# Kernel optimization log

Measured on AMD Instinct MI355X. Metric: run time of the kernel, lower is better.

## Reference

```python
import jax, jax.numpy as jnp
import numpy as np

B, T, I, H, O = 64, 512, 512, 1024, 128
EPS = 1e-5

def _uniform(key, shape, bound):
    return jax.random.uniform(key, shape, jnp.float32, -bound, bound)

def setup_inputs() -> dict:
    key = jax.random.key(0)
    ks = jax.random.split(key, 16)
    bI = 1.0 / np.sqrt(I)
    bH = 1.0 / np.sqrt(H)
    inp = {
        "x": jax.random.normal(ks[0], (B, T, I), jnp.float32),
        # input projection (Linear: y = x @ W.T + b)
        "w_proj": _uniform(ks[1], (H, I), bI),
        "b_proj": _uniform(ks[2], (H,), bI),
        # GRU layer 0 (input_dim -> hidden_dim), PyTorch gate order [r, z, n]
        "w_ih0": _uniform(ks[3], (3 * H, I), bH),
        "w_hh0": _uniform(ks[4], (3 * H, H), bH),
        "b_ih0": _uniform(ks[5], (3 * H,), bH),
        "b_hh0": _uniform(ks[6], (3 * H,), bH),
        # GRU layer 1 (hidden_dim -> hidden_dim)
        "w_ih1": _uniform(ks[7], (3 * H, H), bH),
        "w_hh1": _uniform(ks[8], (3 * H, H), bH),
        "b_ih1": _uniform(ks[9], (3 * H,), bH),
        "b_hh1": _uniform(ks[10], (3 * H,), bH),
        # BatchNorm1d (eval mode: running stats)
        "bn_gamma": jnp.ones((H,), jnp.float32),
        "bn_beta": jnp.zeros((H,), jnp.float32),
        "bn_mean": jnp.zeros((H,), jnp.float32),
        "bn_var": jnp.ones((H,), jnp.float32),
        # output projection
        "w_out": _uniform(ks[11], (O, H), bH),
        "b_out": _uniform(ks[12], (O,), bH),
    }
    return inp

def _gru_layer(x_seq, w_ih, w_hh, b_ih, b_hh):
    """x_seq: [B, T, D_in] -> outputs [B, T, H]. PyTorch GRU gate math."""
    # Precompute input-side gates for all timesteps in one big GEMM.
    gx = jnp.einsum('btd,gd->btg', x_seq, w_ih) + b_ih      # [B, T, 3H]
    gx = jnp.transpose(gx, (1, 0, 2))                        # [T, B, 3H]
    h0 = jnp.zeros((x_seq.shape[0], w_hh.shape[1]), x_seq.dtype)

    def step(h, gx_t):
        gh = h @ w_hh.T + b_hh                               # [B, 3H]
        gxr, gxz, gxn = jnp.split(gx_t, 3, axis=-1)
        ghr, ghz, ghn = jnp.split(gh, 3, axis=-1)
        r = jax.nn.sigmoid(gxr + ghr)
        z = jax.nn.sigmoid(gxz + ghz)
        n = jnp.tanh(gxn + r * ghn)
        h_new = (1.0 - z) * n + z * h
        return h_new, h_new

    _, ys = jax.lax.scan(step, h0, gx)                       # ys: [T, B, H]
    return jnp.transpose(ys, (1, 0, 2))                      # [B, T, H]

def reference(x, w_proj, b_proj,
              w_ih0, w_hh0, b_ih0, b_hh0,
              w_ih1, w_hh1, b_ih1, b_hh1,
              bn_gamma, bn_beta, bn_mean, bn_var,
              w_out, b_out):
    x_projected = x @ w_proj.T + b_proj                      # [B, T, H]
    h1 = _gru_layer(x, w_ih0, w_hh0, b_ih0, b_hh0)           # layer 0
    gru_out = _gru_layer(h1, w_ih1, w_hh1, b_ih1, b_hh1)     # layer 1 (eval: no inter-layer dropout)
    residual = x_projected + gru_out
    out = residual[:, -1, :]                                 # [B, H]
    # BatchNorm1d in eval mode (running stats); dropout is identity in eval.
    out = (out - bn_mean) * jax.lax.rsqrt(bn_var + EPS) * bn_gamma + bn_beta
    out = out @ w_out.T + b_out                              # [B, O]
    return out
```

## Files before the change

### kernel.cpp

```cpp
#include <hip/hip_runtime.h>
#include <math.h>

#define BB 64
#define TT 512
#define II 512
#define HH 1024
#define OO 128
#define GN (3*HH)
#define TC 64
#define NCH (TT/TC)
#define NSLOT 66

using u16 = unsigned short;
typedef __attribute__((ext_vector_type(8))) short bf16x8;
typedef __attribute__((ext_vector_type(4))) float f32x4;
typedef __attribute__((ext_vector_type(4))) unsigned short u16x4;

__device__ __forceinline__ u16 f2bf(float f){
  unsigned u = __builtin_bit_cast(unsigned, f);
  u += 0x7fffu + ((u >> 16) & 1u);
  return (u16)(u >> 16);
}
__device__ __forceinline__ float bf2f(u16 h){
  unsigned u = ((unsigned)h) << 16;
  return __builtin_bit_cast(float, u);
}

__global__ __launch_bounds__(256) void cvt_kernel(const float* __restrict__ s,
                                                  u16* __restrict__ d, int n4){
  int stride = gridDim.x * 256;
  for (int i = blockIdx.x * 256 + threadIdx.x; i < n4; i += stride){
    float4 v = reinterpret_cast<const float4*>(s)[i];
    u16x4 o; o.x = f2bf(v.x); o.y = f2bf(v.y); o.z = f2bf(v.z); o.w = f2bf(v.w);
    reinterpret_cast<u16x4*>(d)[i] = o;
  }
}

__global__ __launch_bounds__(256) void cvtx_chunk(const float* __restrict__ x,
                                                  u16* __restrict__ d, int t0){
  const int per_b = TC * II / 4;
  int stride = gridDim.x * 256;
  for (int i = blockIdx.x * 256 + threadIdx.x; i < BB * per_b; i += stride){
    int b = i / per_b, r = i - b * per_b;
    float4 v = reinterpret_cast<const float4*>(x)[(size_t)(b * TT + t0) * (II/4) + r];
    u16x4 o; o.x = f2bf(v.x); o.y = f2bf(v.y); o.z = f2bf(v.z); o.w = f2bf(v.w);
    reinterpret_cast<u16x4*>(d)[(size_t)b * per_b + r] = o;
  }
}

template<int K>
__global__ __launch_bounds__(256) void gemm_bias(const u16* __restrict__ A,
    const u16* __restrict__ Bw, const float* __restrict__ bias, u16* __restrict__ C){
  __shared__ u16 As[128*32];
  __shared__ u16 Bs[128*32];
  int tid = threadIdx.x;
  int lane = tid & 63, wave = tid >> 6;
  int m0 = blockIdx.x * 128, n0 = blockIdx.y * 128;
  int wr = (wave >> 1) * 64, wc = (wave & 1) * 64;
  int fr = lane & 15, fo = (lane >> 4) * 8;
  f32x4 acc[4][4] = {};
  for (int k0 = 0; k0 < K; k0 += 32){
    __syncthreads();
    #pragma unroll
    for (int c = 0; c < 2; ++c){
      int chunk = wave * 2 + c;
      int s = chunk * 64 + lane;
      int row = s >> 2, o = s & 3;
      const u16* ga = A  + (size_t)(m0 + row) * K + k0 + o * 8;
      const u16* gb = Bw + (size_t)(n0 + row) * K + k0 + o * 8;
      __builtin_amdgcn_global_load_lds(
          (const __attribute__((address_space(1))) unsigned int*)ga,
          (__attribute__((address_space(3))) unsigned int*)(As + chunk * 512), 16, 0, 0);
      __builtin_amdgcn_global_load_lds(
          (const __attribute__((address_space(1))) unsigned int*)gb,
          (__attribute__((address_space(3))) unsigned int*)(Bs + chunk * 512), 16, 0, 0);
    }
    __syncthreads();
    bf16x8 af[4], bf[4];
    #pragma unroll
    for (int m = 0; m < 4; ++m)
      af[m] = *reinterpret_cast<const bf16x8*>(&As[(wr + m*16 + fr) * 32 + fo]);
    #pragma unroll
    for (int n = 0; n < 4; ++n)
      bf[n] = *reinterpret_cast<const bf16x8*>(&Bs[(wc + n*16 + fr) * 32 + fo]);
    #pragma unroll
    for (int m = 0; m < 4; ++m)
      #pragma unroll
      for (int n = 0; n < 4; ++n)
        acc[m][n] = __builtin_amdgcn_mfma_f32_16x16x32_bf16(af[m], bf[n], acc[m][n], 0, 0, 0);
  }
  int r4 = (lane >> 4) * 4;
  #pragma unroll
  for (int n = 0; n < 4; ++n){
    int col = n0 + wc + n*16 + fr;
    float bv = bias[col];
    #pragma unroll
    for (int m = 0; m < 4; ++m){
      #pragma unroll
      for (int q = 0; q < 4; ++q){
        int row = m0 + wr + m*16 + r4 + q;
        C[(size_t)row * GN + col] = f2bf(acc[m][n][q] + bv);
      }
    }
  }
}

__device__ __forceinline__ void gru_chunk(
    const u16* __restrict__ gx, const u16* __restrict__ Whh, const float* __restrict__ bhh,
    u16* hbuf, unsigned* flags, u16* h1c, float* hstate, int base,
    int bl, u16* Ws, float* part, float* bsh)
{
  int tid = threadIdx.x, lane = tid & 63, w = tid >> 6;
  int g = bl >> 6, wg = bl & 63;
  int c0 = wg * 16, rb0 = g * 32;
  for (int ch = tid; ch < 48 * 128; ch += 256){
    int r = ch >> 7, o = ch & 127;
    const u16* src = Whh + (size_t)((r >> 4) * HH + c0 + (r & 15)) * HH + o * 8;
    *reinterpret_cast<int4*>(&Ws[r * 1032 + o * 8]) = *reinterpret_cast<const int4*>(src);
  }
  if (tid < 48) bsh[tid] = bhh[(tid >> 4) * HH + c0 + (tid & 15)];
  __syncthreads();
  int b2 = tid >> 4, j = tid & 15;
  int fr = lane & 15, klo = (lane >> 4) * 8, kw = w * 256;
  const u16* gxp0 = gx + (size_t)(rb0 + b2) * TC * GN + c0 + j;
  const u16* gxp1 = gx + (size_t)(rb0 + 16 + b2) * TC * GN + c0 + j;
  unsigned* fgrp = flags + g * 1024;
  float ho0 = hstate[(size_t)(rb0 + b2) * HH + c0 + j];
  float ho1 = hstate[(size_t)(rb0 + 16 + b2) * HH + c0 + j];
  int lnD = (b2 >> 2) * 16 + j, regD = b2 & 3;
  float br = bhh[c0 + j];
  for (int tl = 0; tl < TC; ++tl){
    int t = base + tl;
    float gxr0 = bf2f(gxp0[(size_t)tl * GN]);
    float gxz0 = bf2f(gxp0[(size_t)tl * GN + HH]);
    float gxn0 = bf2f(gxp0[(size_t)tl * GN + 2 * HH]);
    float gxr1 = bf2f(gxp1[(size_t)tl * GN]);
    float gxz1 = bf2f(gxp1[(size_t)tl * GN + HH]);
    float gxn1 = bf2f(gxp1[(size_t)tl * GN + 2 * HH]);
    if (tl){
      for (;;){
        unsigned v = __hip_atomic_load(fgrp + lane * 16, __ATOMIC_RELAXED,
                                       __HIP_MEMORY_SCOPE_AGENT);
        if (__all((int)(v >= (unsigned)tl))) break;
        __builtin_amdgcn_s_sleep(1);
      }
    }
    asm volatile("" ::: "memory");
    const u16* rslot = hbuf + (size_t)(((t - 1) % 65) + 1) * (BB * HH);
    const u16* hr0 = rslot + (size_t)(rb0 + fr) * HH + kw + klo;
    const u16* hr1 = hr0 + (size_t)16 * HH;
    bf16x8 af0[8], af1[8];
    #pragma unroll
    for (int ks = 0; ks < 8; ++ks){
      af0[ks] = *reinterpret_cast<const bf16x8*>(hr0 + ks * 32);
      af1[ks] = *reinterpret_cast<const bf16x8*>(hr1 + ks * 32);
    }
    f32x4 acc[2][3] = {};
    #pragma unroll
    for (int ks = 0; ks < 8; ++ks){
      int kk = kw + ks * 32 + klo;
      bf16x8 w0 = *reinterpret_cast<const bf16x8*>(&Ws[(      fr) * 1032 + kk]);
      bf16x8 w1 = *reinterpret_cast<const bf16x8*>(&Ws[(16 + fr) * 1032 + kk]);
      bf16x8 w2 = *reinterpret_cast<const bf16x8*>(&Ws[(32 + fr) * 1032 + kk]);
      acc[0][0] = __builtin_amdgcn_mfma_f32_16x16x32_bf16(af0[ks], w0, acc[0][0], 0, 0, 0);
      acc[0][1] = __builtin_amdgcn_mfma_f32_16x16x32_bf16(af0[ks], w1, acc[0][1], 0, 0, 0);
      acc[0][2] = __builtin_amdgcn_mfma_f32_16x16x32_bf16(af0[ks], w2, acc[0][2], 0, 0, 0);
      acc[1][0] = __builtin_amdgcn_mfma_f32_16x16x32_bf16(af1[ks], w0, acc[1][0], 0, 0, 0);
      acc[1][1] = __builtin_amdgcn_mfma_f32_16x16x32_bf16(af1[ks], w1, acc[1][1], 0, 0, 0);
      acc[1][2] = __builtin_amdgcn_mfma_f32_16x16x32_bf16(af1[ks], w2, acc[1][2], 0, 0, 0);
    }
    #pragma unroll
    for (int at = 0; at < 2; ++at)
      #pragma unroll
      for (int gt = 0; gt < 3; ++gt)
        *reinterpret_cast<f32x4*>(&part[((w*6 + at*3 + gt)*64 + lane)*4]) = acc[at][gt];
    __syncthreads();
    float gh[2][3];
    #pragma unroll
    for (int at = 0; at < 2; ++at)
      #pragma unroll
      for (int gt = 0; gt < 3; ++gt){
        float s = 0.f;
        #pragma unroll
        for (int ww = 0; ww < 4; ++ww)
          s += part[((ww*6 + at*3 + gt)*64 + lnD)*4 + regD];
        gh[at][gt] = s;
      }
    float bz = bsh[16 + j], bn2 = bsh[32 + j];
    float r0 = __builtin_amdgcn_rcpf(1.f + __expf(-(gxr0 + gh[0][0] + br)));
    float z0 = __builtin_amdgcn_rcpf(1.f + __expf(-(gxz0 + gh[0][1] + bz)));
    float nx0 = gxn0 + r0 * (gh[0][2] + bn2);
    float n0 = 1.f - 2.f * __builtin_amdgcn_rcpf(__expf(2.f * nx0) + 1.f);
    float hn0 = (1.f - z0) * n0 + z0 * ho0;
    float r1 = __builtin_amdgcn_rcpf(1.f + __expf(-(gxr1 + gh[1][0] + br)));
    float z1 = __builtin_amdgcn_rcpf(1.f + __expf(-(gxz1 + gh[1][1] + bz)));
    float nx1 = gxn1 + r1 * (gh[1][2] + bn2);
    float n1 = 1.f - 2.f * __builtin_amdgcn_rcpf(__expf(2.f * nx1) + 1.f);
    float hn1 = (1.f - z1) * n1 + z1 * ho1;
    ho0 = hn0; ho1 = hn1;
    u16 hb0 = f2bf(hn0), hb1 = f2bf(hn1);
    u16* wslot = hbuf + (size_t)((t % 65) + 1) * (BB * HH);
    size_t d0 = (size_t)(rb0 + b2) * HH + c0 + j;
    __hip_atomic_store(wslot + d0,                hb0, __ATOMIC_RELAXED, __HIP_MEMORY_SCOPE_AGENT);
    __hip_atomic_store(wslot + d0 + (size_t)16*HH, hb1, __ATOMIC_RELAXED, __HIP_MEMORY_SCOPE_AGENT);
    if (h1c){
      h1c[((size_t)(rb0 + b2) * TC + tl) * HH + c0 + j] = hb0;
      h1c[((size_t)(rb0 + 16 + b2) * TC + tl) * HH + c0 + j] = hb1;
    }
    if (tl == TC - 1){
      hstate[(size_t)(rb0 + b2) * HH + c0 + j] = hn0;
      hstate[(size_t)(rb0 + 16 + b2) * HH + c0 + j] = hn1;
    }
    __syncthreads();
    if (tid == 0)
      __hip_atomic_store(fgrp + wg * 16, (unsigned)(tl + 1), __ATOMIC_RELAXED,
                         __HIP_MEMORY_SCOPE_AGENT);
  }
}

__global__ __launch_bounds__(256, 1) void gru_fused(
    const u16* gxA, const u16* WhhA, const float* bhhA, u16* hbufA,
    unsigned* flA, u16* h1cA, float* hstA, int baseA,
    const u16* gxB, const u16* WhhB, const float* bhhB, u16* hbufB,
    unsigned* flB, float* hstB, int baseB)
{
  __shared__ u16 Ws[48 * 1032];
  __shared__ float part[4*6*64*4];
  __shared__ float bsh[48];
  int blk = blockIdx.x;
  if (blk < 128){
    if (!gxA) return;
    gru_chunk(gxA, WhhA, bhhA, hbufA, flA, h1cA, hstA, baseA, blk, Ws, part, bsh);
  } else {
    if (!gxB) return;
    gru_chunk(gxB, WhhB, bhhB, hbufB, flB, nullptr, hstB, baseB, blk - 128, Ws, part, bsh);
  }
}

__global__ __launch_bounds__(256) void xproj_kernel(const float* __restrict__ x,
    const float* __restrict__ wproj, const float* __restrict__ bproj, float* __restrict__ xp){
  __shared__ float xs[II];
  int b = blockIdx.x >> 2, n0 = (blockIdx.x & 3) << 8;
  const float* xrow = x + ((size_t)b * TT + (TT - 1)) * II;
  for (int i = threadIdx.x; i < II; i += 256) xs[i] = xrow[i];
  __syncthreads();
  int n = n0 + threadIdx.x;
  const float* wrow = wproj + (size_t)n * II;
  float s = 0.f;
  #pragma unroll 4
  for (int k = 0; k < II; k += 4){
    float4 w4 = *reinterpret_cast<const float4*>(&wrow[k]);
    s += xs[k]*w4.x + xs[k+1]*w4.y + xs[k+2]*w4.z + xs[k+3]*w4.w;
  }
  xp[(size_t)b * HH + n] = s + bproj[n];
}

__global__ __launch_bounds__(256) void final_kernel(const float* __restrict__ xp,
    const float* __restrict__ hl, const float* __restrict__ gamma, const float* __restrict__ beta,
    const float* __restrict__ mean, const float* __restrict__ var,
    const float* __restrict__ wout, const float* __restrict__ bout, float* __restrict__ out){
  __shared__ float bn[2 * HH];
  int b0 = blockIdx.x * 2;
  for (int i = threadIdx.x; i < 2 * HH; i += 256){
    int bb = i >> 10, jj = i & (HH - 1);
    float res = xp[(size_t)(b0 + bb) * HH + jj] + hl[(size_t)(b0 + bb) * HH + jj];
    bn[i] = (res - mean[jj]) * rsqrtf(var[jj] + 1e-5f) * gamma[jj] + beta[jj];
  }
  __syncthreads();
  int bb = threadIdx.x >> 7, o = threadIdx.x & (OO - 1);
  const float* wrow = wout + (size_t)o * HH;
  const float* bnrow = bn + bb * HH;
  float s = 0.f;
  #pragma unroll 4
  for (int k = 0; k < HH; k += 4){
    float4 w4 = *reinterpret_cast<const float4*>(&wrow[k]);
    s += bnrow[k]*w4.x + bnrow[k+1]*w4.y + bnrow[k+2]*w4.z + bnrow[k+3]*w4.w;
  }
  out[(size_t)(b0 + bb) * OO + o] = s + bout[o];
}

extern "C" void kernel_launch(void* const* d_in, const int* in_sizes, int n_in,
                              void* d_out, int out_size, void* d_ws, size_t ws_size,
                              hipStream_t stream) {
  const float* x      = (const float*)d_in[0];
  const float* w_proj = (const float*)d_in[1];
  const float* b_proj = (const float*)d_in[2];
  const float* w_ih0  = (const float*)d_in[3];
  const float* w_hh0  = (const float*)d_in[4];
  const float* b_ih0  = (const float*)d_in[5];
  const float* b_hh0  = (const float*)d_in[6];
  const float* w_ih1  = (const float*)d_in[7];
  const float* w_hh1  = (const float*)d_in[8];
  const float* b_ih1  = (const float*)d_in[9];
  const float* b_hh1  = (const float*)d_in[10];
  const float* gamma  = (const float*)d_in[11];
  const float* beta   = (const float*)d_in[12];
  const float* mean   = (const float*)d_in[13];
  const float* var    = (const float*)d_in[14];
  const float* w_out  = (const float*)d_in[15];
  const float* b_out  = (const float*)d_in[16];
  float* out = (float*)d_out;

  char* ws = (char*)d_ws;
  size_t off = 0;
  unsigned* flags = (unsigned*)(ws + off); off += (size_t)18 * 2048 * 4;
  float* hst0  = (float*)(ws + off); off += (size_t)BB*HH*4;
  float* hst1  = (float*)(ws + off); off += (size_t)BB*HH*4;
  size_t zeroA = off;
  u16* hbuf0   = (u16*)(ws + off);   off += (size_t)NSLOT*BB*HH*2;
  u16* hbuf1   = (u16*)(ws + off);   off += (size_t)NSLOT*BB*HH*2;
  float* xproj = (float*)(ws + off); off += (size_t)BB*HH*4;
  u16* xck     = (u16*)(ws + off);   off += (size_t)BB*TC*II*2;
  u16* h1c     = (u16*)(ws + off);   off += (size_t)BB*TC*HH*2;
  u16* wih0b   = (u16*)(ws + off);   off += (size_t)3*HH*II*2;
  u16* whh0b   = (u16*)(ws + off);   off += (size_t)3*HH*HH*2;
  u16* wih1b   = (u16*)(ws + off);   off += (size_t)3*HH*HH*2;
  u16* whh1b   = (u16*)(ws + off);   off += (size_t)3*HH*HH*2;
  u16* gxc0    = (u16*)(ws + off);   off += (size_t)BB*TC*3*HH*2;
  u16* gxc1    = (u16*)(ws + off);   off += (size_t)BB*TC*3*HH*2;

  hipMemsetAsync(d_ws, 0, zeroA, stream);
  hipMemsetAsync(hbuf0, 0, (size_t)BB*HH*2, stream);
  hipMemsetAsync(hbuf1, 0, (size_t)BB*HH*2, stream);

  cvt_kernel<<<512, 256, 0, stream>>>(w_ih0, wih0b, (3*HH*II) / 4);
  cvt_kernel<<<512, 256, 0, stream>>>(w_hh0, whh0b, (3*HH*HH) / 4);
  cvt_kernel<<<512, 256, 0, stream>>>(w_ih1, wih1b, (3*HH*HH) / 4);
  cvt_kernel<<<512, 256, 0, stream>>>(w_hh1, whh1b, (3*HH*HH) / 4);

  xproj_kernel<<<256, 256, 0, stream>>>(x, w_proj, b_proj, xproj);

  dim3 ggrid(BB * TC / 128, GN / 128);
  auto fl = [&](int k, int role){ return flags + (size_t)(k*2 + role) * 2048; };

  cvtx_chunk<<<1024, 256, 0, stream>>>(x, xck, 0);
  gemm_bias<II><<<ggrid, 256, 0, stream>>>(xck, wih0b, b_ih0, gxc0);
  gru_fused<<<256, 256, 0, stream>>>(gxc0, whh0b, b_hh0, hbuf0, fl(0,0), h1c, hst0, 0,
                                     nullptr, whh1b, b_hh1, hbuf1, fl(0,1), hst1, 0);
  for (int k = 1; k < NCH; ++k){
    gemm_bias<HH><<<ggrid, 256, 0, stream>>>(h1c, wih1b, b_ih1, gxc1);
    cvtx_chunk<<<1024, 256, 0, stream>>>(x, xck, k * TC);
    gemm_bias<II><<<ggrid, 256, 0, stream>>>(xck, wih0b, b_ih0, gxc0);
    gru_fused<<<256, 256, 0, stream>>>(gxc0, whh0b, b_hh0, hbuf0, fl(k,0), h1c, hst0, k*TC,
                                       gxc1, whh1b, b_hh1, hbuf1, fl(k,1), hst1, (k-1)*TC);
  }
  gemm_bias<HH><<<ggrid, 256, 0, stream>>>(h1c, wih1b, b_ih1, gxc1);
  gru_fused<<<256, 256, 0, stream>>>(nullptr, whh0b, b_hh0, hbuf0, fl(8,0), h1c, hst0, 0,
                                     gxc1, whh1b, b_hh1, hbuf1, fl(8,1), hst1, (NCH-1)*TC);

  final_kernel<<<BB / 2, 256, 0, stream>>>(xproj, hst1, gamma, beta, mean, var, w_out, b_out, out);
}
```

Before: 3.070 ms.

## Replace per-step flag handshake with parity bits embedded in hidden-state data

```diff
diff --git a/kernel.cpp b/kernel.cpp
--- a/kernel.cpp
+++ b/kernel.cpp
@@ -9,12 +9,16 @@
 #define GN (3*HH)
 #define TC 64
 #define NCH (TT/TC)
-#define NSLOT 66
+#define NSLOT 65
 
 using u16 = unsigned short;
 typedef __attribute__((ext_vector_type(8))) short bf16x8;
 typedef __attribute__((ext_vector_type(4))) float f32x4;
 typedef __attribute__((ext_vector_type(4))) unsigned short u16x4;
+typedef __attribute__((ext_vector_type(2))) unsigned long long u64x2;
+
+#define PARMASK64 0x0001000100010001ULL
+#define KEEPMASK64 0xFFFEFFFEFFFEFFFEULL
 
 __device__ __forceinline__ u16 f2bf(float f){
   unsigned u = __builtin_bit_cast(unsigned, f);
@@ -33,6 +37,18 @@
     float4 v = reinterpret_cast<const float4*>(s)[i];
     u16x4 o; o.x = f2bf(v.x); o.y = f2bf(v.y); o.z = f2bf(v.z); o.w = f2bf(v.w);
     reinterpret_cast<u16x4*>(d)[i] = o;
+  }
+}
+
+__global__ __launch_bounds__(256) void hinit_kernel(unsigned long long* hb0,
+                                                    unsigned long long* hb1){
+  const int wper = BB * HH / 4;
+  int stride = gridDim.x * 256;
+  for (int i = blockIdx.x * 256 + threadIdx.x; i < NSLOT * wper; i += stride){
+    int s = i / wper;
+    unsigned long long v = ((s & 1) ^ 1) ? PARMASK64 : 0ULL;
+    __hip_atomic_store(hb0 + i, v, __ATOMIC_RELAXED, __HIP_MEMORY_SCOPE_AGENT);
+    __hip_atomic_store(hb1 + i, v, __ATOMIC_RELAXED, __HIP_MEMORY_SCOPE_AGENT);
   }
 }
 
@@ -107,8 +123,8 @@
 
 __device__ __forceinline__ void gru_chunk(
     const u16* __restrict__ gx, const u16* __restrict__ Whh, const float* __restrict__ bhh,
-    u16* hbuf, unsigned* flags, u16* h1c, float* hstate, int base,
-    int bl, u16* Ws, float* part, float* bsh)
+    u16* hbuf, u16* h1c, float* hstate, int base,
+    int bl, u16* Ws, float* part, u16* hlds, float* bsh)
 {
   int tid = threadIdx.x, lane = tid & 63, w = tid >> 6;
   int g = bl >> 6, wg = bl & 63;
@@ -124,11 +140,12 @@
   int fr = lane & 15, klo = (lane >> 4) * 8, kw = w * 256;
   const u16* gxp0 = gx + (size_t)(rb0 + b2) * TC * GN + c0 + j;
   const u16* gxp1 = gx + (size_t)(rb0 + 16 + b2) * TC * GN + c0 + j;
-  unsigned* fgrp = flags + g * 1024;
   float ho0 = hstate[(size_t)(rb0 + b2) * HH + c0 + j];
   float ho1 = hstate[(size_t)(rb0 + 16 + b2) * HH + c0 + j];
   int lnD = (b2 >> 2) * 16 + j, regD = b2 & 3;
   float br = bhh[c0 + j];
+  int rr = tid >> 3, pp = tid & 7;
+  const int SLOTW = BB * HH / 2;
   for (int tl = 0; tl < TC; ++tl){
     int t = base + tl;
     float gxr0 = bf2f(gxp0[(size_t)tl * GN]);
@@ -137,23 +154,59 @@
     float gxr1 = bf2f(gxp1[(size_t)tl * GN]);
     float gxz1 = bf2f(gxp1[(size_t)tl * GN + HH]);
     float gxn1 = bf2f(gxp1[(size_t)tl * GN + 2 * HH]);
-    if (tl){
+    bf16x8 af0[8], af1[8];
+    if (t == 0){
+      u64x2 z; z.x = 0; z.y = 0;
+      #pragma unroll
+      for (int ks = 0; ks < 8; ++ks){ af0[ks] = __builtin_bit_cast(bf16x8, z);
+                                      af1[ks] = __builtin_bit_cast(bf16x8, z); }
+    } else {
+      const unsigned long long want = ((t - 1) & 1) ? PARMASK64 : 0ULL;
+      const unsigned* rs = (const unsigned*)hbuf + (size_t)((t - 1) % NSLOT) * SLOTW;
+      const unsigned* ba0 = rs + (size_t)(rb0 + fr) * 512 + ((kw + klo) >> 1);
+      const unsigned* ba1 = ba0 + 16 * 512;
+      unsigned long long vlo[2][8], vhi[2][8];
+      #pragma unroll
+      for (int ks = 0; ks < 8; ++ks){
+        vlo[0][ks] = __hip_atomic_load((const unsigned long long*)(ba0 + ks*16),
+                                       __ATOMIC_RELAXED, __HIP_MEMORY_SCOPE_AGENT);
+        vhi[0][ks] = __hip_atomic_load((const unsigned long long*)(ba0 + ks*16 + 2),
+                                       __ATOMIC_RELAXED, __HIP_MEMORY_SCOPE_AGENT);
+        vlo[1][ks] = __hip_atomic_load((const unsigned long long*)(ba1 + ks*16),
+                                       __ATOMIC_RELAXED, __HIP_MEMORY_SCOPE_AGENT);
+        vhi[1][ks] = __hip_atomic_load((const unsigned long long*)(ba1 + ks*16 + 2),
+                                       __ATOMIC_RELAXED, __HIP_MEMORY_SCOPE_AGENT);
+      }
       for (;;){
-        unsigned v = __hip_atomic_load(fgrp + lane * 16, __ATOMIC_RELAXED,
-                                       __HIP_MEMORY_SCOPE_AGENT);
-        if (__all((int)(v >= (unsigned)tl))) break;
-        __builtin_amdgcn_s_sleep(1);
+        unsigned pend = 0;
+        #pragma unroll
+        for (int a = 0; a < 2; ++a)
+          #pragma unroll
+          for (int ks = 0; ks < 8; ++ks){
+            if ((vlo[a][ks] & PARMASK64) != want) pend |= 1u << (a*8 + ks);
+            if ((vhi[a][ks] & PARMASK64) != want) pend |= 1u << (16 + a*8 + ks);
+          }
+        if (__all((int)(pend == 0u))) break;
+        #pragma unroll
+        for (int a = 0; a < 2; ++a)
+          #pragma unroll
+          for (int ks = 0; ks < 8; ++ks){
+            const unsigned* bb = (a ? ba1 : ba0) + ks*16;
+            if (pend & (1u << (a*8 + ks)))
+              vlo[a][ks] = __hip_atomic_load((const unsigned long long*)bb,
+                                             __ATOMIC_RELAXED, __HIP_MEMORY_SCOPE_AGENT);
+            if (pend & (1u << (16 + a*8 + ks)))
+              vhi[a][ks] = __hip_atomic_load((const unsigned long long*)(bb + 2),
+                                             __ATOMIC_RELAXED, __HIP_MEMORY_SCOPE_AGENT);
+          }
       }
-    }
-    asm volatile("" ::: "memory");
-    const u16* rslot = hbuf + (size_t)(((t - 1) % 65) + 1) * (BB * HH);
-    const u16* hr0 = rslot + (size_t)(rb0 + fr) * HH + kw + klo;
-    const u16* hr1 = hr0 + (size_t)16 * HH;
-    bf16x8 af0[8], af1[8];
-    #pragma unroll
-    for (int ks = 0; ks < 8; ++ks){
-      af0[ks] = *reinterpret_cast<const bf16x8*>(hr0 + ks * 32);
-      af1[ks] = *reinterpret_cast<const bf16x8*>(hr1 + ks * 32);
+      #pragma unroll
+      for (int ks = 0; ks < 8; ++ks){
+        u64x2 p0; p0.x = vlo[0][ks] & KEEPMASK64; p0.y = vhi[0][ks] & KEEPMASK64;
+        af0[ks] = __builtin_bit_cast(bf16x8, p0);
+        u64x2 p1; p1.x = vlo[1][ks] & KEEPMASK64; p1.y = vhi[1][ks] & KEEPMASK64;
+        af1[ks] = __builtin_bit_cast(bf16x8, p1);
+      }
     }
     f32x4 acc[2][3] = {};
     #pragma unroll
@@ -199,10 +252,14 @@
     float hn1 = (1.f - z1) * n1 + z1 * ho1;
     ho0 = hn0; ho1 = hn1;
     u16 hb0 = f2bf(hn0), hb1 = f2bf(hn1);
-    u16* wslot = hbuf + (size_t)((t % 65) + 1) * (BB * HH);
-    size_t d0 = (size_t)(rb0 + b2) * HH + c0 + j;
-    __hip_atomic_store(wslot + d0,                hb0, __ATOMIC_RELAXED, __HIP_MEMORY_SCOPE_AGENT);
-    __hip_atomic_store(wslot + d0 + (size_t)16*HH, hb1, __ATOMIC_RELAXED, __HIP_MEMORY_SCOPE_AGENT);
+    hlds[b2 * 16 + j] = hb0;
+    hlds[(16 + b2) * 16 + j] = hb1;
+    __syncthreads();
+    unsigned pk = (unsigned)hlds[rr*16 + pp*2] | ((unsigned)hlds[rr*16 + pp*2 + 1] << 16);
+    pk = (pk & 0xFFFEFFFEu) | ((t & 1) ? 0x00010001u : 0u);
+    __hip_atomic_store((unsigned*)hbuf + (size_t)(t % NSLOT) * SLOTW
+                         + (size_t)(rb0 + rr) * 512 + (c0 >> 1) + pp,
+                       pk, __ATOMIC_RELAXED, __HIP_MEMORY_SCOPE_AGENT);
     if (h1c){
       h1c[((size_t)(rb0 + b2) * TC + tl) * HH + c0 + j] = hb0;
       h1c[((size_t)(rb0 + 16 + b2) * TC + tl) * HH + c0 + j] = hb1;
@@ -211,29 +268,26 @@
       hstate[(size_t)(rb0 + b2) * HH + c0 + j] = hn0;
       hstate[(size_t)(rb0 + 16 + b2) * HH + c0 + j] = hn1;
     }
-    __syncthreads();
-    if (tid == 0)
-      __hip_atomic_store(fgrp + wg * 16, (unsigned)(tl + 1), __ATOMIC_RELAXED,
-                         __HIP_MEMORY_SCOPE_AGENT);
   }
 }
 
 __global__ __launch_bounds__(256, 1) void gru_fused(
     const u16* gxA, const u16* WhhA, const float* bhhA, u16* hbufA,
-    unsigned* flA, u16* h1cA, float* hstA, int baseA,
+    u16* h1cA, float* hstA, int baseA,
     const u16* gxB, const u16* WhhB, const float* bhhB, u16* hbufB,
-    unsigned* flB, float* hstB, int baseB)
+    float* hstB, int baseB)
 {
   __shared__ u16 Ws[48 * 1032];
   __shared__ float part[4*6*64*4];
+  __shared__ u16 hlds[32 * 16];
   __shared__ float bsh[48];
   int blk = blockIdx.x;
   if (blk < 128){
     if (!gxA) return;
-    gru_chunk(gxA, WhhA, bhhA, hbufA, flA, h1cA, hstA, baseA, blk, Ws, part, bsh);
+    gru_chunk(gxA, WhhA, bhhA, hbufA, h1cA, hstA, baseA, blk, Ws, part, hlds, bsh);
   } else {
     if (!gxB) return;
-    gru_chunk(gxB, WhhB, bhhB, hbufB, flB, nullptr, hstB, baseB, blk - 128, Ws, part, bsh);
+    gru_chunk(gxB, WhhB, bhhB, hbufB, nullptr, hstB, baseB, blk - 128, Ws, part, hlds, bsh);
   }
 }
 
@@ -303,7 +357,6 @@
 
   char* ws = (char*)d_ws;
   size_t off = 0;
-  unsigned* flags = (unsigned*)(ws + off); off += (size_t)18 * 2048 * 4;
   float* hst0  = (float*)(ws + off); off += (size_t)BB*HH*4;
   float* hst1  = (float*)(ws + off); off += (size_t)BB*HH*4;
   size_t zeroA = off;
@@ -320,8 +373,8 @@
   u16* gxc1    = (u16*)(ws + off);   off += (size_t)BB*TC*3*HH*2;
 
   hipMemsetAsync(d_ws, 0, zeroA, stream);
-  hipMemsetAsync(hbuf0, 0, (size_t)BB*HH*2, stream);
-  hipMemsetAsync(hbuf1, 0, (size_t)BB*HH*2, stream);
+  hinit_kernel<<<2048, 256, 0, stream>>>((unsigned long long*)hbuf0,
+                                         (unsigned long long*)hbuf1);
 
   cvt_kernel<<<512, 256, 0, stream>>>(w_ih0, wih0b, (3*HH*II) / 4);
   cvt_kernel<<<512, 256, 0, stream>>>(w_hh0, whh0b, (3*HH*HH) / 4);
@@ -331,22 +384,21 @@
   xproj_kernel<<<256, 256, 0, stream>>>(x, w_proj, b_proj, xproj);
 
   dim3 ggrid(BB * TC / 128, GN / 128);
-  auto fl = [&](int k, int role){ return flags + (size_t)(k*2 + role) * 2048; };
 
   cvtx_chunk<<<1024, 256, 0, stream>>>(x, xck, 0);
   gemm_bias<II><<<ggrid, 256, 0, stream>>>(xck, wih0b, b_ih0, gxc0);
-  gru_fused<<<256, 256, 0, stream>>>(gxc0, whh0b, b_hh0, hbuf0, fl(0,0), h1c, hst0, 0,
-                                     nullptr, whh1b, b_hh1, hbuf1, fl(0,1), hst1, 0);
+  gru_fused<<<256, 256, 0, stream>>>(gxc0, whh0b, b_hh0, hbuf0, h1c, hst0, 0,
+                                     nullptr, whh1b, b_hh1, hbuf1, hst1, 0);
   for (int k = 1; k < NCH; ++k){
     gemm_bias<HH><<<ggrid, 256, 0, stream>>>(h1c, wih1b, b_ih1, gxc1);
     cvtx_chunk<<<1024, 256, 0, stream>>>(x, xck, k * TC);
     gemm_bias<II><<<ggrid, 256, 0, stream>>>(xck, wih0b, b_ih0, gxc0);
-    gru_fused<<<256, 256, 0, stream>>>(gxc0, whh0b, b_hh0, hbuf0, fl(k,0), h1c, hst0, k*TC,
-                                       gxc1, whh1b, b_hh1, hbuf1, fl(k,1), hst1, (k-1)*TC);
+    gru_fused<<<256, 256, 0, stream>>>(gxc0, whh0b, b_hh0, hbuf0, h1c, hst0, k*TC,
+                                       gxc1, whh1b, b_hh1, hbuf1, hst1, (k-1)*TC);
   }
   gemm_bias<HH><<<ggrid, 256, 0, stream>>>(h1c, wih1b, b_ih1, gxc1);
-  gru_fused<<<256, 256, 0, stream>>>(nullptr, whh0b, b_hh0, hbuf0, fl(8,0), h1c, hst0, 0,
-                                     gxc1, whh1b, b_hh1, hbuf1, fl(8,1), hst1, (NCH-1)*TC);
+  gru_fused<<<256, 256, 0, stream>>>(nullptr, whh0b, b_hh0, hbuf0, h1c, hst0, 0,
+                                     gxc1, whh1b, b_hh1, hbuf1, hst1, (NCH-1)*TC);
 
   final_kernel<<<BB / 2, 256, 0, stream>>>(xproj, hst1, gamma, beta, mean, var, w_out, b_out, out);
 }
```

New measurement: 4.201 ms. 1.37x slower.

## Split GRU recurrence per-wave with full-K MFMA and per-wave flags, dropping block barriers

Applied to the files above, without the earlier changes.

```diff
diff --git a/kernel.cpp b/kernel.cpp
--- a/kernel.cpp
+++ b/kernel.cpp
@@ -9,7 +9,7 @@
 #define GN (3*HH)
 #define TC 64
 #define NCH (TT/TC)
-#define NSLOT 66
+#define NSLOT 65
 
 using u16 = unsigned short;
 typedef __attribute__((ext_vector_type(8))) short bf16x8;
@@ -108,132 +108,108 @@
 __device__ __forceinline__ void gru_chunk(
     const u16* __restrict__ gx, const u16* __restrict__ Whh, const float* __restrict__ bhh,
     u16* hbuf, unsigned* flags, u16* h1c, float* hstate, int base,
-    int bl, u16* Ws, float* part, float* bsh)
+    int bl, u16* Ws)
 {
   int tid = threadIdx.x, lane = tid & 63, w = tid >> 6;
-  int g = bl >> 6, wg = bl & 63;
-  int c0 = wg * 16, rb0 = g * 32;
-  for (int ch = tid; ch < 48 * 128; ch += 256){
+  int grp = bl >> 6, wg = bl & 63;
+  int c0 = wg * 16, rb0 = grp * 32;
+  for (int ch = tid; ch < 48 * 128; ch += 128){
     int r = ch >> 7, o = ch & 127;
     const u16* src = Whh + (size_t)((r >> 4) * HH + c0 + (r & 15)) * HH + o * 8;
     *reinterpret_cast<int4*>(&Ws[r * 1032 + o * 8]) = *reinterpret_cast<const int4*>(src);
   }
-  if (tid < 48) bsh[tid] = bhh[(tid >> 4) * HH + c0 + (tid & 15)];
   __syncthreads();
-  int b2 = tid >> 4, j = tid & 15;
-  int fr = lane & 15, klo = (lane >> 4) * 8, kw = w * 256;
-  const u16* gxp0 = gx + (size_t)(rb0 + b2) * TC * GN + c0 + j;
-  const u16* gxp1 = gx + (size_t)(rb0 + 16 + b2) * TC * GN + c0 + j;
-  unsigned* fgrp = flags + g * 1024;
-  float ho0 = hstate[(size_t)(rb0 + b2) * HH + c0 + j];
-  float ho1 = hstate[(size_t)(rb0 + 16 + b2) * HH + c0 + j];
-  int lnD = (b2 >> 2) * 16 + j, regD = b2 & 3;
-  float br = bhh[c0 + j];
+  int fr = lane & 15, klo = (lane >> 4) * 8, r4 = (lane >> 4) * 4;
+  int myrow0 = rb0 + w * 16;
+  float br = bhh[c0 + fr], bz = bhh[HH + c0 + fr], bn2 = bhh[2*HH + c0 + fr];
+  float ho[4];
+  #pragma unroll
+  for (int q = 0; q < 4; ++q)
+    ho[q] = hstate[(size_t)(myrow0 + r4 + q) * HH + c0 + fr];
+  unsigned* myflag = flags + ((grp * 64 + wg) * 2 + w) * 16;
+  const unsigned* pollbase = flags + (grp * 64 + lane) * 2 * 16 + w * 16;
   for (int tl = 0; tl < TC; ++tl){
     int t = base + tl;
-    float gxr0 = bf2f(gxp0[(size_t)tl * GN]);
-    float gxz0 = bf2f(gxp0[(size_t)tl * GN + HH]);
-    float gxn0 = bf2f(gxp0[(size_t)tl * GN + 2 * HH]);
-    float gxr1 = bf2f(gxp1[(size_t)tl * GN]);
-    float gxz1 = bf2f(gxp1[(size_t)tl * GN + HH]);
-    float gxn1 = bf2f(gxp1[(size_t)tl * GN + 2 * HH]);
-    if (tl){
+    float gr[4], gz[4], gn[4];
+    #pragma unroll
+    for (int q = 0; q < 4; ++q){
+      const u16* gp = gx + (size_t)(myrow0 + r4 + q) * TC * GN + (size_t)tl * GN + c0 + fr;
+      gr[q] = bf2f(gp[0]); gz[q] = bf2f(gp[HH]); gn[q] = bf2f(gp[2*HH]);
+    }
+    f32x4 accR = {}, accZ = {}, accN = {};
+    if (t){
+      unsigned want = (unsigned)t;
       for (;;){
-        unsigned v = __hip_atomic_load(fgrp + lane * 16, __ATOMIC_RELAXED,
+        unsigned v = __hip_atomic_load(pollbase, __ATOMIC_RELAXED,
                                        __HIP_MEMORY_SCOPE_AGENT);
-        if (__all((int)(v >= (unsigned)tl))) break;
+        if (__all((int)(v >= want))) break;
         __builtin_amdgcn_s_sleep(1);
       }
-    }
-    asm volatile("" ::: "memory");
-    const u16* rslot = hbuf + (size_t)(((t - 1) % 65) + 1) * (BB * HH);
-    const u16* hr0 = rslot + (size_t)(rb0 + fr) * HH + kw + klo;
-    const u16* hr1 = hr0 + (size_t)16 * HH;
-    bf16x8 af0[8], af1[8];
-    #pragma unroll
-    for (int ks = 0; ks < 8; ++ks){
-      af0[ks] = *reinterpret_cast<const bf16x8*>(hr0 + ks * 32);
-      af1[ks] = *reinterpret_cast<const bf16x8*>(hr1 + ks * 32);
-    }
-    f32x4 acc[2][3] = {};
-    #pragma unroll
-    for (int ks = 0; ks < 8; ++ks){
-      int kk = kw + ks * 32 + klo;
-      bf16x8 w0 = *reinterpret_cast<const bf16x8*>(&Ws[(      fr) * 1032 + kk]);
-      bf16x8 w1 = *reinterpret_cast<const bf16x8*>(&Ws[(16 + fr) * 1032 + kk]);
-      bf16x8 w2 = *reinterpret_cast<const bf16x8*>(&Ws[(32 + fr) * 1032 + kk]);
-      acc[0][0] = __builtin_amdgcn_mfma_f32_16x16x32_bf16(af0[ks], w0, acc[0][0], 0, 0, 0);
-      acc[0][1] = __builtin_amdgcn_mfma_f32_16x16x32_bf16(af0[ks], w1, acc[0][1], 0, 0, 0);
-      acc[0][2] = __builtin_amdgcn_mfma_f32_16x16x32_bf16(af0[ks], w2, acc[0][2], 0, 0, 0);
-      acc[1][0] = __builtin_amdgcn_mfma_f32_16x16x32_bf16(af1[ks], w0, acc[1][0], 0, 0, 0);
-      acc[1][1] = __builtin_amdgcn_mfma_f32_16x16x32_bf16(af1[ks], w1, acc[1][1], 0, 0, 0);
-      acc[1][2] = __builtin_amdgcn_mfma_f32_16x16x32_bf16(af1[ks], w2, acc[1][2], 0, 0, 0);
-    }
-    #pragma unroll
-    for (int at = 0; at < 2; ++at)
-      #pragma unroll
-      for (int gt = 0; gt < 3; ++gt)
-        *reinterpret_cast<f32x4*>(&part[((w*6 + at*3 + gt)*64 + lane)*4]) = acc[at][gt];
-    __syncthreads();
-    float gh[2][3];
-    #pragma unroll
-    for (int at = 0; at < 2; ++at)
-      #pragma unroll
-      for (int gt = 0; gt < 3; ++gt){
-        float s = 0.f;
-        #pragma unroll
-        for (int ww = 0; ww < 4; ++ww)
-          s += part[((ww*6 + at*3 + gt)*64 + lnD)*4 + regD];
-        gh[at][gt] = s;
+      asm volatile("" ::: "memory");
+      const u16* hr = hbuf + (size_t)((t - 1) % NSLOT) * (BB * HH)
+                    + (size_t)(myrow0 + fr) * HH + klo;
+      bf16x8 af[32];
+      #pragma unroll
+      for (int ks = 0; ks < 32; ++ks)
+        af[ks] = *reinterpret_cast<const bf16x8*>(hr + ks * 32);
+      #pragma unroll
+      for (int ks = 0; ks < 32; ++ks){
+        int kk = ks * 32 + klo;
+        bf16x8 w0 = *reinterpret_cast<const bf16x8*>(&Ws[(     fr) * 1032 + kk]);
+        bf16x8 w1 = *reinterpret_cast<const bf16x8*>(&Ws[(16 + fr) * 1032 + kk]);
+        bf16x8 w2 = *reinterpret_cast<const bf16x8*>(&Ws[(32 + fr) * 1032 + kk]);
+        accR = __builtin_amdgcn_mfma_f32_16x16x32_bf16(af[ks], w0, accR, 0, 0, 0);
+        accZ = __builtin_amdgcn_mfma_f32_16x16x32_bf16(af[ks], w1, accZ, 0, 0, 0);
+        accN = __builtin_amdgcn_mfma_f32_16x16x32_bf16(af[ks], w2, accN, 0, 0, 0);
       }
-    float bz = bsh[16 + j], bn2 = bsh[32 + j];
-    float r0 = __builtin_amdgcn_rcpf(1.f + __expf(-(gxr0 + gh[0][0] + br)));
-    float z0 = __builtin_amdgcn_rcpf(1.f + __expf(-(gxz0 + gh[0][1] + bz)));
-    float nx0 = gxn0 + r0 * (gh[0][2] + bn2);
-    float n0 = 1.f - 2.f * __builtin_amdgcn_rcpf(__expf(2.f * nx0) + 1.f);
-    float hn0 = (1.f - z0) * n0 + z0 * ho0;
-    float r1 = __builtin_amdgcn_rcpf(1.f + __expf(-(gxr1 + gh[1][0] + br)));
-    float z1 = __builtin_amdgcn_rcpf(1.f + __expf(-(gxz1 + gh[1][1] + bz)));
-    float nx1 = gxn1 + r1 * (gh[1][2] + bn2);
-    float n1 = 1.f - 2.f * __builtin_amdgcn_rcpf(__expf(2.f * nx1) + 1.f);
-    float hn1 = (1.f - z1) * n1 + z1 * ho1;
-    ho0 = hn0; ho1 = hn1;
-    u16 hb0 = f2bf(hn0), hb1 = f2bf(hn1);
-    u16* wslot = hbuf + (size_t)((t % 65) + 1) * (BB * HH);
-    size_t d0 = (size_t)(rb0 + b2) * HH + c0 + j;
-    __hip_atomic_store(wslot + d0,                hb0, __ATOMIC_RELAXED, __HIP_MEMORY_SCOPE_AGENT);
-    __hip_atomic_store(wslot + d0 + (size_t)16*HH, hb1, __ATOMIC_RELAXED, __HIP_MEMORY_SCOPE_AGENT);
+    }
+    u16 hb[4]; float hn[4];
+    #pragma unroll
+    for (int q = 0; q < 4; ++q){
+      float r_ = __builtin_amdgcn_rcpf(1.f + __expf(-(gr[q] + accR[q] + br)));
+      float z_ = __builtin_amdgcn_rcpf(1.f + __expf(-(gz[q] + accZ[q] + bz)));
+      float nx = gn[q] + r_ * (accN[q] + bn2);
+      float n_ = 1.f - 2.f * __builtin_amdgcn_rcpf(__expf(2.f * nx) + 1.f);
+      hn[q] = (1.f - z_) * n_ + z_ * ho[q];
+      ho[q] = hn[q];
+      hb[q] = f2bf(hn[q]);
+    }
+    u16* wslot = hbuf + (size_t)(t % NSLOT) * (BB * HH);
+    #pragma unroll
+    for (int q = 0; q < 4; ++q)
+      __hip_atomic_store(wslot + (size_t)(myrow0 + r4 + q) * HH + c0 + fr,
+                         hb[q], __ATOMIC_RELAXED, __HIP_MEMORY_SCOPE_AGENT);
+    asm volatile("s_waitcnt vmcnt(0)" ::: "memory");
+    if (lane == 0)
+      __hip_atomic_store(myflag, (unsigned)(t + 1), __ATOMIC_RELAXED,
+                         __HIP_MEMORY_SCOPE_AGENT);
     if (h1c){
-      h1c[((size_t)(rb0 + b2) * TC + tl) * HH + c0 + j] = hb0;
-      h1c[((size_t)(rb0 + 16 + b2) * TC + tl) * HH + c0 + j] = hb1;
+      #pragma unroll
+      for (int q = 0; q < 4; ++q)
+        h1c[((size_t)(myrow0 + r4 + q) * TC + tl) * HH + c0 + fr] = hb[q];
     }
     if (tl == TC - 1){
-      hstate[(size_t)(rb0 + b2) * HH + c0 + j] = hn0;
-      hstate[(size_t)(rb0 + 16 + b2) * HH + c0 + j] = hn1;
-    }
-    __syncthreads();
-    if (tid == 0)
-      __hip_atomic_store(fgrp + wg * 16, (unsigned)(tl + 1), __ATOMIC_RELAXED,
-                         __HIP_MEMORY_SCOPE_AGENT);
-  }
-}
-
-__global__ __launch_bounds__(256, 1) void gru_fused(
+      #pragma unroll
+      for (int q = 0; q < 4; ++q)
+        hstate[(size_t)(myrow0 + r4 + q) * HH + c0 + fr] = hn[q];
+    }
+  }
+}
+
+__global__ __launch_bounds__(128, 1) void gru_fused(
     const u16* gxA, const u16* WhhA, const float* bhhA, u16* hbufA,
     unsigned* flA, u16* h1cA, float* hstA, int baseA,
     const u16* gxB, const u16* WhhB, const float* bhhB, u16* hbufB,
     unsigned* flB, float* hstB, int baseB)
 {
   __shared__ u16 Ws[48 * 1032];
-  __shared__ float part[4*6*64*4];
-  __shared__ float bsh[48];
   int blk = blockIdx.x;
   if (blk < 128){
     if (!gxA) return;
-    gru_chunk(gxA, WhhA, bhhA, hbufA, flA, h1cA, hstA, baseA, blk, Ws, part, bsh);
+    gru_chunk(gxA, WhhA, bhhA, hbufA, flA, h1cA, hstA, baseA, blk, Ws);
   } else {
     if (!gxB) return;
-    gru_chunk(gxB, WhhB, bhhB, hbufB, flB, nullptr, hstB, baseB, blk - 128, Ws, part, bsh);
+    gru_chunk(gxB, WhhB, bhhB, hbufB, flB, nullptr, hstB, baseB, blk - 128, Ws);
   }
 }
 
@@ -303,7 +279,8 @@
 
   char* ws = (char*)d_ws;
   size_t off = 0;
-  unsigned* flags = (unsigned*)(ws + off); off += (size_t)18 * 2048 * 4;
+  unsigned* flA  = (unsigned*)(ws + off); off += (size_t)2*64*2*16*4;
+  unsigned* flB  = (unsigned*)(ws + off); off += (size_t)2*64*2*16*4;
   float* hst0  = (float*)(ws + off); off += (size_t)BB*HH*4;
   float* hst1  = (float*)(ws + off); off += (size_t)BB*HH*4;
   size_t zeroA = off;
@@ -320,8 +297,6 @@
   u16* gxc1    = (u16*)(ws + off);   off += (size_t)BB*TC*3*HH*2;
 
   hipMemsetAsync(d_ws, 0, zeroA, stream);
-  hipMemsetAsync(hbuf0, 0, (size_t)BB*HH*2, stream);
-  hipMemsetAsync(hbuf1, 0, (size_t)BB*HH*2, stream);
 
   cvt_kernel<<<512, 256, 0, stream>>>(w_ih0, wih0b, (3*HH*II) / 4);
   cvt_kernel<<<512, 256, 0, stream>>>(w_hh0, whh0b, (3*HH*HH) / 4);
@@ -331,22 +306,21 @@
   xproj_kernel<<<256, 256, 0, stream>>>(x, w_proj, b_proj, xproj);
 
   dim3 ggrid(BB * TC / 128, GN / 128);
-  auto fl = [&](int k, int role){ return flags + (size_t)(k*2 + role) * 2048; };
 
   cvtx_chunk<<<1024, 256, 0, stream>>>(x, xck, 0);
   gemm_bias<II><<<ggrid, 256, 0, stream>>>(xck, wih0b, b_ih0, gxc0);
-  gru_fused<<<256, 256, 0, stream>>>(gxc0, whh0b, b_hh0, hbuf0, fl(0,0), h1c, hst0, 0,
-                                     nullptr, whh1b, b_hh1, hbuf1, fl(0,1), hst1, 0);
+  gru_fused<<<256, 128, 0, stream>>>(gxc0, whh0b, b_hh0, hbuf0, flA, h1c, hst0, 0,
+                                     nullptr, whh1b, b_hh1, hbuf1, flB, hst1, 0);
   for (int k = 1; k < NCH; ++k){
     gemm_bias<HH><<<ggrid, 256, 0, stream>>>(h1c, wih1b, b_ih1, gxc1);
     cvtx_chunk<<<1024, 256, 0, stream>>>(x, xck, k * TC);
     gemm_bias<II><<<ggrid, 256, 0, stream>>>(xck, wih0b, b_ih0, gxc0);
-    gru_fused<<<256, 256, 0, stream>>>(gxc0, whh0b, b_hh0, hbuf0, fl(k,0), h1c, hst0, k*TC,
-                                       gxc1, whh1b, b_hh1, hbuf1, fl(k,1), hst1, (k-1)*TC);
+    gru_fused<<<256, 128, 0, stream>>>(gxc0, whh0b, b_hh0, hbuf0, flA, h1c, hst0, k*TC,
+                                       gxc1, whh1b, b_hh1, hbuf1, flB, hst1, (k-1)*TC);
   }
   gemm_bias<HH><<<ggrid, 256, 0, stream>>>(h1c, wih1b, b_ih1, gxc1);
-  gru_fused<<<256, 256, 0, stream>>>(nullptr, whh0b, b_hh0, hbuf0, fl(8,0), h1c, hst0, 0,
-                                     gxc1, whh1b, b_hh1, hbuf1, fl(8,1), hst1, (NCH-1)*TC);
+  gru_fused<<<256, 128, 0, stream>>>(nullptr, whh0b, b_hh0, hbuf0, flA, h1c, hst0, 0,
+                                     gxc1, whh1b, b_hh1, hbuf1, flB, hst1, (NCH-1)*TC);
 
   final_kernel<<<BB / 2, 256, 0, stream>>>(xproj, hst1, gamma, beta, mean, var, w_out, b_out, out);
 }
```

Result: slower. 5.283 ms (+72.1%).

## Overlap next-chunk layer-0 input GEMM with GRU recurrence in extra warps

Applied to the files above, without the earlier changes.

```diff
diff --git a/kernel.cpp b/kernel.cpp
--- a/kernel.cpp
+++ b/kernel.cpp
@@ -10,6 +10,7 @@
 #define TC 64
 #define NCH (TT/TC)
 #define NSLOT 66
+#define NBAR 129
 
 using u16 = unsigned short;
 typedef __attribute__((ext_vector_type(8))) short bf16x8;
@@ -218,22 +219,70 @@
   }
 }
 
-__global__ __launch_bounds__(256, 1) void gru_fused(
+__device__ __forceinline__ void role_c_gemm(
+    const float* __restrict__ x, const u16* __restrict__ Wih,
+    const float* __restrict__ bih, u16* __restrict__ dst, int t0c, int gw)
+{
+  int lane = threadIdx.x & 63;
+  int fr = lane & 15, klo = (lane >> 4) * 8, r4 = (lane >> 4) * 4;
+  bool hasC = (t0c < TT) && (dst != nullptr);
+  int done = 0;
+  for (int it = 0; it < NBAR; ++it){
+    if (hasC && done < 48 && (it == 0 || (it & 1))){
+      int tile = gw * 48 + done; ++done;
+      int tm = tile / 192, tn = tile - tm * 192;
+      int m0 = tm * 16, n0 = tn * 16;
+      int mrow = m0 + fr;
+      int b = mrow >> 6, tl = mrow & 63;
+      const float* xr = x + ((size_t)b * TT + t0c + tl) * II + klo;
+      const u16* br = Wih + (size_t)(n0 + fr) * II + klo;
+      f32x4 acc = {};
+      #pragma unroll
+      for (int ks = 0; ks < 16; ++ks){
+        float4 a0 = *reinterpret_cast<const float4*>(xr + ks * 32);
+        float4 a1 = *reinterpret_cast<const float4*>(xr + ks * 32 + 4);
+        u16x4 p0, p1;
+        p0.x = f2bf(a0.x); p0.y = f2bf(a0.y); p0.z = f2bf(a0.z); p0.w = f2bf(a0.w);
+        p1.x = f2bf(a1.x); p1.y = f2bf(a1.y); p1.z = f2bf(a1.z); p1.w = f2bf(a1.w);
+        struct { u16x4 lo, hi; } packed{p0, p1};
+        bf16x8 af = __builtin_bit_cast(bf16x8, packed);
+        bf16x8 bf = *reinterpret_cast<const bf16x8*>(br + ks * 32);
+        acc = __builtin_amdgcn_mfma_f32_16x16x32_bf16(af, bf, acc, 0, 0, 0);
+      }
+      float bv = bih[n0 + fr];
+      #pragma unroll
+      for (int q = 0; q < 4; ++q)
+        dst[(size_t)(m0 + r4 + q) * GN + (n0 + fr)] = f2bf(acc[q] + bv);
+    }
+    __syncthreads();
+  }
+}
+
+__global__ __launch_bounds__(512, 1) void gru_fused(
     const u16* gxA, const u16* WhhA, const float* bhhA, u16* hbufA,
     unsigned* flA, u16* h1cA, float* hstA, int baseA,
     const u16* gxB, const u16* WhhB, const float* bhhB, u16* hbufB,
-    unsigned* flB, float* hstB, int baseB)
+    unsigned* flB, float* hstB, int baseB,
+    const float* x, const u16* wihC, const float* bihC, u16* gxoutC, int t0c)
 {
   __shared__ u16 Ws[48 * 1032];
   __shared__ float part[4*6*64*4];
   __shared__ float bsh[48];
+  int tid = threadIdx.x;
   int blk = blockIdx.x;
-  if (blk < 128){
-    if (!gxA) return;
-    gru_chunk(gxA, WhhA, bhhA, hbufA, flA, h1cA, hstA, baseA, blk, Ws, part, bsh);
+  if (tid < 256){
+    const u16* gx = (blk < 128) ? gxA : gxB;
+    if (gx){
+      if (blk < 128)
+        gru_chunk(gxA, WhhA, bhhA, hbufA, flA, h1cA, hstA, baseA, blk, Ws, part, bsh);
+      else
+        gru_chunk(gxB, WhhB, bhhB, hbufB, flB, nullptr, hstB, baseB, blk - 128, Ws, part, bsh);
+    } else {
+      for (int i = 0; i < NBAR; ++i) __syncthreads();
+    }
   } else {
-    if (!gxB) return;
-    gru_chunk(gxB, WhhB, bhhB, hbufB, flB, nullptr, hstB, baseB, blk - 128, Ws, part, bsh);
+    int gw = blk * 4 + ((tid >> 6) - 4);
+    role_c_gemm(x, wihC, bihC, gxoutC, t0c, gw);
   }
 }
 
@@ -310,14 +359,15 @@
   u16* hbuf0   = (u16*)(ws + off);   off += (size_t)NSLOT*BB*HH*2;
   u16* hbuf1   = (u16*)(ws + off);   off += (size_t)NSLOT*BB*HH*2;
   float* xproj = (float*)(ws + off); off += (size_t)BB*HH*4;
-  u16* xck     = (u16*)(ws + off);   off += (size_t)BB*TC*II*2;
   u16* h1c     = (u16*)(ws + off);   off += (size_t)BB*TC*HH*2;
   u16* wih0b   = (u16*)(ws + off);   off += (size_t)3*HH*II*2;
   u16* whh0b   = (u16*)(ws + off);   off += (size_t)3*HH*HH*2;
   u16* wih1b   = (u16*)(ws + off);   off += (size_t)3*HH*HH*2;
   u16* whh1b   = (u16*)(ws + off);   off += (size_t)3*HH*HH*2;
-  u16* gxc0    = (u16*)(ws + off);   off += (size_t)BB*TC*3*HH*2;
   u16* gxc1    = (u16*)(ws + off);   off += (size_t)BB*TC*3*HH*2;
+  u16* gxc0a   = (u16*)(ws + off);   off += (size_t)BB*TC*3*HH*2;
+  u16* gxc0b   = (u16*)(ws + off);   off += (size_t)BB*TC*3*HH*2;
+  u16* xck     = gxc0b;
 
   hipMemsetAsync(d_ws, 0, zeroA, stream);
   hipMemsetAsync(hbuf0, 0, (size_t)BB*HH*2, stream);
@@ -332,21 +382,23 @@
 
   dim3 ggrid(BB * TC / 128, GN / 128);
   auto fl = [&](int k, int role){ return flags + (size_t)(k*2 + role) * 2048; };
+  u16* gxc0[2] = { gxc0a, gxc0b };
 
   cvtx_chunk<<<1024, 256, 0, stream>>>(x, xck, 0);
-  gemm_bias<II><<<ggrid, 256, 0, stream>>>(xck, wih0b, b_ih0, gxc0);
-  gru_fused<<<256, 256, 0, stream>>>(gxc0, whh0b, b_hh0, hbuf0, fl(0,0), h1c, hst0, 0,
-                                     nullptr, whh1b, b_hh1, hbuf1, fl(0,1), hst1, 0);
+  gemm_bias<II><<<ggrid, 256, 0, stream>>>(xck, wih0b, b_ih0, gxc0[0]);
+  gru_fused<<<256, 512, 0, stream>>>(gxc0[0], whh0b, b_hh0, hbuf0, fl(0,0), h1c, hst0, 0,
+                                     nullptr, whh1b, b_hh1, hbuf1, fl(0,1), hst1, 0,
+                                     x, wih0b, b_ih0, gxc0[1], TC);
   for (int k = 1; k < NCH; ++k){
     gemm_bias<HH><<<ggrid, 256, 0, stream>>>(h1c, wih1b, b_ih1, gxc1);
-    cvtx_chunk<<<1024, 256, 0, stream>>>(x, xck, k * TC);
-    gemm_bias<II><<<ggrid, 256, 0, stream>>>(xck, wih0b, b_ih0, gxc0);
-    gru_fused<<<256, 256, 0, stream>>>(gxc0, whh0b, b_hh0, hbuf0, fl(k,0), h1c, hst0, k*TC,
-                                       gxc1, whh1b, b_hh1, hbuf1, fl(k,1), hst1, (k-1)*TC);
+    gru_fused<<<256, 512, 0, stream>>>(gxc0[k & 1], whh0b, b_hh0, hbuf0, fl(k,0), h1c, hst0, k*TC,
+                                       gxc1, whh1b, b_hh1, hbuf1, fl(k,1), hst1, (k-1)*TC,
+                                       x, wih0b, b_ih0, gxc0[(k + 1) & 1], (k + 1) * TC);
   }
   gemm_bias<HH><<<ggrid, 256, 0, stream>>>(h1c, wih1b, b_ih1, gxc1);
-  gru_fused<<<256, 256, 0, stream>>>(nullptr, whh0b, b_hh0, hbuf0, fl(8,0), h1c, hst0, 0,
-                                     gxc1, whh1b, b_hh1, hbuf1, fl(8,1), hst1, (NCH-1)*TC);
+  gru_fused<<<256, 512, 0, stream>>>(nullptr, whh0b, b_hh0, hbuf0, fl(8,0), h1c, hst0, 0,
+                                     gxc1, whh1b, b_hh1, hbuf1, fl(8,1), hst1, (NCH-1)*TC,
+                                     x, wih0b, b_ih0, nullptr, TT);
 
   final_kernel<<<BB / 2, 256, 0, stream>>>(xproj, hst1, gamma, beta, mean, var, w_out, b_out, out);
 }
```

After: 4.365 ms. 1.42x slower.
